# Performance work log

Hardware: AMD Instinct MI355X
Metric: run time of the kernel (lower is better)

Reference implementation:

```python
import jax, jax.numpy as jnp
import numpy as np

B, N, M, C1, C2, H = 16, 4096, 1024, 256, 512, 256
SE_C = max(1, int(H / 24.0))  # 10
BN_EPS = 1e-5

def _bn(x, g, b):
    # training-mode BatchNorm over (B, n) per channel; x: [B, C, n]
    mean = jnp.mean(x, axis=(0, 2), keepdims=True)
    var = jnp.mean((x - mean) ** 2, axis=(0, 2), keepdims=True)  # biased var (torch)
    return (x - mean) * jax.lax.rsqrt(var + BN_EPS) * g[None, :, None] + b[None, :, None]

def _swish(x):
    return x * jax.nn.sigmoid(x)

def setup_inputs() -> dict:
    key = jax.random.key(0)
    ks = jax.random.split(key, 12)
    d = {
        "unknown": jax.random.normal(ks[0], (B, N, 3), jnp.float32),
        "known": jax.random.normal(ks[1], (B, M, 3), jnp.float32),
        "unknow_feats": jax.random.normal(ks[2], (B, C1, N), jnp.float32),
        "known_feats": jax.random.normal(ks[3], (B, C2, M), jnp.float32),
        # conv1 (C1+C2 -> H), no bias (bn)
        "W1": jax.random.normal(ks[4], (H, C1 + C2), jnp.float32) * (1.0 / np.sqrt(C1 + C2)),
        "g1": jnp.ones((H,), jnp.float32),
        "b1": jnp.zeros((H,), jnp.float32),
        # SE block (1x1 convs with bias, no pooling in this impl)
        "se_rw": jax.random.normal(ks[5], (SE_C, H), jnp.float32) * (1.0 / np.sqrt(H)),
        "se_rb": jnp.zeros((SE_C,), jnp.float32),
        "se_ew": jax.random.normal(ks[6], (H, SE_C), jnp.float32) * (1.0 / np.sqrt(SE_C)),
        "se_eb": jnp.zeros((H,), jnp.float32),
        # conv2 (H -> H), no bias
        "W2": jax.random.normal(ks[7], (H, H), jnp.float32) * (1.0 / np.sqrt(H)),
        "g2": jnp.ones((H,), jnp.float32),
        "b2": jnp.zeros((H,), jnp.float32),
    }
    return d

def reference(unknown, known, unknow_feats, known_feats,
              W1, g1, b1, se_rw, se_rb, se_ew, se_eb, W2, g2, b2):
    # three_nn: squared distances of each unknown point to all known points
    d2 = jnp.sum((unknown[:, :, None, :] - known[:, None, :, :]) ** 2, axis=-1)  # [B,N,M]
    neg_d, idx = jax.lax.top_k(-d2, 3)  # 3 smallest
    dist = -neg_d                                       # [B,N,3]
    dist_recip = 1.0 / (dist + 1e-8)
    weight = dist_recip / jnp.sum(dist_recip, axis=2, keepdims=True)  # [B,N,3]
    # three_interpolate: gather known_feats at idx, inverse-distance weighted sum
    gathered = jnp.take_along_axis(known_feats[:, :, None, :], idx[:, None, :, :], axis=3)  # [B,C2,N,3]
    interp = jnp.sum(gathered * weight[:, None, :, :], axis=-1)  # [B,C2,N]
    x = jnp.concatenate([interp, unknow_feats], axis=1)  # [B,C1+C2,N]
    # conv1 (1x1) + BN + SE
    h = jnp.einsum('oc,bcn->bon', W1, x)
    h = _bn(h, g1, b1)
    s = jnp.einsum('oc,bcn->bon', se_rw, h) + se_rb[None, :, None]
    s = _swish(s)
    s = jnp.einsum('oc,bcn->bon', se_ew, s) + se_eb[None, :, None]
    h = jax.nn.sigmoid(s) * h
    # conv2 (1x1) + BN + ReLU
    h = jnp.einsum('oc,bcn->bon', W2, h)
    h = _bn(h, g2, b2)
    return jax.nn.relu(h)  # [B, H, N]
```

## Files before the change

kernel.cpp:

```cpp
#include <hip/hip_runtime.h>
#include <math.h>

#define B_ 16
#define N_ 4096
#define M_ 1024
#define C1_ 256
#define C2_ 512
#define H_ 256
#define SEC_ 10
#define OC_ 8
#define BN_EPS 1e-5f

typedef _Float16 f16;
typedef f16 f16x8 __attribute__((ext_vector_type(8)));
typedef f16 f16x4 __attribute__((ext_vector_type(4)));
typedef f16 f16x2 __attribute__((ext_vector_type(2)));
typedef float f32x4 __attribute__((ext_vector_type(4)));

__global__ __launch_bounds__(256)
void three_nn_kernel(const float* __restrict__ unknown, const float* __restrict__ known,
                     int* __restrict__ idxp, float* __restrict__ wgtp)
{
    __shared__ float kx[M_], ky[M_], kz[M_];
    __shared__ float cd[4][64][3];
    __shared__ int   ci[4][64][3];
    const int b  = blockIdx.y;
    const int bn = blockIdx.x * 64;
    const int t  = threadIdx.x;
    const float* kb = known + (long)b * M_ * 3;

    {
        const float4 q0 = *(const float4*)(kb + 12*t);
        const float4 q1 = *(const float4*)(kb + 12*t + 4);
        const float4 q2 = *(const float4*)(kb + 12*t + 8);
        const int m = 4*t;
        kx[m+0]=q0.x; ky[m+0]=q0.y; kz[m+0]=q0.z;
        kx[m+1]=q0.w; ky[m+1]=q1.x; kz[m+1]=q1.y;
        kx[m+2]=q1.z; ky[m+2]=q1.w; kz[m+2]=q2.x;
        kx[m+3]=q2.y; ky[m+3]=q2.z; kz[m+3]=q2.w;
    }
    __syncthreads();

    const int w = t >> 6, ln = t & 63;
    const int n = bn + ln;
    const float* up = unknown + ((long)b * N_ + n) * 3;
    const float ux = up[0], uy = up[1], uz = up[2];

    float b0 = 1e30f, b1v = 1e30f, b2v = 1e30f;
    int j0 = 0, j1 = 0, j2 = 0;

    const int m0 = w * 256;
    for (int m = m0; m < m0 + 256; m += 4) {
        const float4 X = *(const float4*)&kx[m];
        const float4 Y = *(const float4*)&ky[m];
        const float4 Z = *(const float4*)&kz[m];
        const float px[4] = {X.x, X.y, X.z, X.w};
        const float py[4] = {Y.x, Y.y, Y.z, Y.w};
        const float pz[4] = {Z.x, Z.y, Z.z, Z.w};
        #pragma unroll
        for (int q = 0; q < 4; q++) {
            const float dx = ux - px[q], dy = uy - py[q], dz = uz - pz[q];
            const float d = dx*dx + dy*dy + dz*dz;
            if (d < b2v) {
                const int mm = m + q;
                if (d < b1v) {
                    b2v = b1v; j2 = j1;
                    if (d < b0) { b1v = b0; j1 = j0; b0 = d; j0 = mm; }
                    else        { b1v = d;  j1 = mm; }
                } else { b2v = d; j2 = mm; }
            }
        }
    }
    cd[w][ln][0] = b0;  cd[w][ln][1] = b1v; cd[w][ln][2] = b2v;
    ci[w][ln][0] = j0;  ci[w][ln][1] = j1;  ci[w][ln][2] = j2;
    __syncthreads();

    if (t < 64) {
        float d0 = cd[0][t][0], d1 = cd[0][t][1], d2 = cd[0][t][2];
        int   i0 = ci[0][t][0], i1 = ci[0][t][1], i2 = ci[0][t][2];
        #pragma unroll
        for (int c = 1; c < 4; c++) {
            #pragma unroll
            for (int j = 0; j < 3; j++) {
                const float d = cd[c][t][j];
                const int  ix = ci[c][t][j];
                if (d < d2) {
                    if (d < d1) {
                        d2 = d1; i2 = i1;
                        if (d < d0) { d1 = d0; i1 = i0; d0 = d; i0 = ix; }
                        else        { d1 = d;  i1 = ix; }
                    } else { d2 = d; i2 = ix; }
                }
            }
        }
        const float r0 = 1.f/(d0 + 1e-8f), r1 = 1.f/(d1 + 1e-8f), r2 = 1.f/(d2 + 1e-8f);
        const float rs = 1.f/(r0 + r1 + r2);
        const long base = ((long)b * N_ + bn + t) * 3;
        idxp[base+0] = i0; idxp[base+1] = i1; idxp[base+2] = i2;
        wgtp[base+0] = r0*rs; wgtp[base+1] = r1*rs; wgtp[base+2] = r2*rs;
    }
}

template<int MODE>
__global__ __launch_bounds__(256)
void gemm_mfma(const float* __restrict__ A, int lda,
               const float* __restrict__ Bf, const f16* __restrict__ Bh,
               long strideB, int ldb, int K,
               f16* __restrict__ Ch, long strideC, int ldc,
               const f16* __restrict__ Gt,
               const int* __restrict__ idxp, const float* __restrict__ wgtp,
               float* __restrict__ psum,
               const float* __restrict__ spart, const float* __restrict__ rbAdj,
               const float* __restrict__ se_ewp, const float* __restrict__ se_ebp,
               const float* __restrict__ a1p, const float* __restrict__ c1p)
{
    __shared__ __align__(16) f16 As[256*72];
    __shared__ __align__(16) f16 Bs[64*72];
    __shared__ float sswl[SEC_*64];

    const int b   = blockIdx.z;
    const int bn  = blockIdx.x * 64;
    const int tid = threadIdx.x;
    const int l = tid & 63, w = tid >> 6;
    const int lane16 = l & 15, quad = l >> 4;

    const float* Bfb = nullptr;
    const f16*   Bhb = nullptr;
    if constexpr (MODE == 2) Bhb = Bh + (long)b*strideB;
    else                     Bfb = Bf + (long)b*strideB;

    if constexpr (MODE == 2) {
        for (int i = tid; i < SEC_*64; i += 256) {
            const int j = i >> 6, nn = i & 63;
            float v = rbAdj[j];
            #pragma unroll
            for (int oc = 0; oc < OC_; oc++)
                v += spart[(((long)oc*B_ + b)*SEC_ + j)*N_ + bn + nn];
            sswl[j*64 + nn] = v / (1.f + __expf(-v));
        }
        __syncthreads();
    }

    f32x4 acc[4][4];
    #pragma unroll
    for (int i = 0; i < 4; i++)
        #pragma unroll
        for (int j = 0; j < 4; j++)
            acc[i][j] = (f32x4){0.f, 0.f, 0.f, 0.f};

    const int akb = (tid & 3) * 16;
    const int arw = tid >> 2;

    for (int k0 = 0; k0 < K; k0 += 64) {
        #pragma unroll
        for (int p = 0; p < 4; p++) {
            const int r = p*64 + arw;
            const float* src = A + (long)r*lda + k0 + akb;
            const float4 v0 = *(const float4*)(src);
            const float4 v1 = *(const float4*)(src + 4);
            const float4 v2 = *(const float4*)(src + 8);
            const float4 v3 = *(const float4*)(src + 12);
            f16x8 h0, h1;
            h0[0]=(f16)v0.x; h0[1]=(f16)v0.y; h0[2]=(f16)v0.z; h0[3]=(f16)v0.w;
            h0[4]=(f16)v1.x; h0[5]=(f16)v1.y; h0[6]=(f16)v1.z; h0[7]=(f16)v1.w;
            h1[0]=(f16)v2.x; h1[1]=(f16)v2.y; h1[2]=(f16)v2.z; h1[3]=(f16)v2.w;
            h1[4]=(f16)v3.x; h1[5]=(f16)v3.y; h1[6]=(f16)v3.z; h1[7]=(f16)v3.w;
            *(f16x8*)&As[r*72 + akb]     = h0;
            *(f16x8*)&As[r*72 + akb + 8] = h1;
        }
        #pragma unroll
        for (int it = 0; it < 2; it++) {
            const int slot = it*256 + tid;
            const int k2 = slot >> 4;
            const int n0 = (slot & 15) * 4;
            if constexpr (MODE == 2) {
                const int ka = k0 + 2*k2;
                const f16* s0 = Bhb + (long)ka*ldb + bn + n0;
                const f16x4 ua = *(const f16x4*)s0;
                const f16x4 ub = *(const f16x4*)(s0 + ldb);
                float val[2][4];
                #pragma unroll
                for (int r = 0; r < 2; r++) {
                    const int kr = ka + r;
                    const float aa = a1p[kr], cc = c1p[kr], eb = se_ebp[kr];
                    const float* ew = se_ewp + kr*SEC_;
                    #pragma unroll
                    for (int j = 0; j < 4; j++) {
                        float e = eb;
                        #pragma unroll
                        for (int q = 0; q < SEC_; q++) e += ew[q]*sswl[q*64 + n0 + j];
                        const float g  = 1.f/(1.f + __expf(-e));
                        const float hv = (r == 0) ? (float)ua[j] : (float)ub[j];
                        val[r][j] = g * (aa*hv + cc);
                    }
                }
                #pragma unroll
                for (int j = 0; j < 4; j++) {
                    f16x2 p; p[0] = (f16)val[0][j]; p[1] = (f16)val[1][j];
                    *(f16x2*)&Bs[(n0+j)*72 + 2*k2] = p;
                }
            } else {
                const float* s0 = Bfb + (long)(k0 + 2*k2)*ldb + bn + n0;
                const float4 u = *(const float4*)s0;
                const float4 v = *(const float4*)(s0 + ldb);
                f16x2 p0, p1, p2, p3;
                p0[0]=(f16)u.x; p0[1]=(f16)v.x;
                p1[0]=(f16)u.y; p1[1]=(f16)v.y;
                p2[0]=(f16)u.z; p2[1]=(f16)v.z;
                p3[0]=(f16)u.w; p3[1]=(f16)v.w;
                *(f16x2*)&Bs[(n0+0)*72 + 2*k2] = p0;
                *(f16x2*)&Bs[(n0+1)*72 + 2*k2] = p1;
                *(f16x2*)&Bs[(n0+2)*72 + 2*k2] = p2;
                *(f16x2*)&Bs[(n0+3)*72 + 2*k2] = p3;
            }
        }
        __syncthreads();
        const int abase = (w*64 + lane16)*72 + quad*8;
        const int bbase = lane16*72 + quad*8;
        #pragma unroll
        for (int s = 0; s < 2; s++) {
            f16x8 af[4], bf[4];
            #pragma unroll
            for (int i = 0; i < 4; i++) af[i] = *(const f16x8*)&As[abase + i*1152 + s*32];
            #pragma unroll
            for (int j = 0; j < 4; j++) bf[j] = *(const f16x8*)&Bs[bbase + j*1152 + s*32];
            #pragma unroll
            for (int i = 0; i < 4; i++)
                #pragma unroll
                for (int j = 0; j < 4; j++)
                    acc[i][j] = __builtin_amdgcn_mfma_f32_16x16x32_f16(af[i], bf[j], acc[i][j], 0, 0, 0);
        }
        __syncthreads();
    }

    if constexpr (MODE == 0) {
        f16* Gl = As;
        #pragma unroll
        for (int i = 0; i < 4; i++)
            #pragma unroll
            for (int r = 0; r < 4; r++) {
                const int h = w*64 + i*16 + quad*4 + r;
                #pragma unroll
                for (int j = 0; j < 4; j++)
                    Gl[(j*16 + lane16)*264 + h] = (f16)acc[i][j][r];
            }
        __syncthreads();
        f16* Gtb = Ch + (long)b*strideC + (long)bn*H_;
        #pragma unroll
        for (int it = 0; it < 8; it++) {
            const int t = it*256 + tid;
            const int m = t >> 5, c = (t & 31)*8;
            *(f16x8*)&Gtb[m*H_ + c] = *(const f16x8*)&Gl[m*264 + c];
        }
    } else {
        if constexpr (MODE == 1) {
            f16* P = As;
            const int p  = tid >> 2;
            const int qd = tid & 3;
            const long ib = ((long)b*N_ + bn + p)*3;
            const int i0 = idxp[ib], i1 = idxp[ib+1], i2 = idxp[ib+2];
            const float w0 = wgtp[ib], w1 = wgtp[ib+1], w2 = wgtp[ib+2];
            const f16* gb = Gt + (long)b*M_*H_;
            const f16* g0 = gb + (long)i0*H_ + qd*64;
            const f16* g1 = gb + (long)i1*H_ + qd*64;
            const f16* g2 = gb + (long)i2*H_ + qd*64;
            f16* Pr = P + p*264 + qd*64;
            #pragma unroll
            for (int c = 0; c < 64; c += 8) {
                const f16x8 x0 = *(const f16x8*)&g0[c];
                const f16x8 x1 = *(const f16x8*)&g1[c];
                const f16x8 x2 = *(const f16x8*)&g2[c];
                f16x8 o;
                #pragma unroll
                for (int e = 0; e < 8; e++)
                    o[e] = (f16)(w0*(float)x0[e] + w1*(float)x1[e] + w2*(float)x2[e]);
                *(f16x8*)&Pr[c] = o;
            }
            __syncthreads();
            #pragma unroll
            for (int i = 0; i < 4; i++)
                #pragma unroll
                for (int r = 0; r < 4; r++) {
                    const int h = w*64 + i*16 + quad*4 + r;
                    #pragma unroll
                    for (int j = 0; j < 4; j++)
                        acc[i][j][r] += (float)P[(j*16 + lane16)*264 + h];
                }
        }
        const int bid = blockIdx.z * gridDim.x + blockIdx.x;
        float* ps = psum + (long)bid * (2*H_);
        f16* Cb = Ch + (long)b*strideC;
        #pragma unroll
        for (int i = 0; i < 4; i++)
            #pragma unroll
            for (int r = 0; r < 4; r++) {
                const int row = w*64 + i*16 + quad*4 + r;
                float s1 = 0.f, s2 = 0.f;
                #pragma unroll
                for (int j = 0; j < 4; j++) {
                    const float v = acc[i][j][r];
                    s1 += v; s2 += v*v;
                    Cb[(long)row*ldc + bn + j*16 + lane16] = (f16)v;
                }
                #pragma unroll
                for (int off = 1; off < 16; off <<= 1) {
                    s1 += __shfl_xor(s1, off, 64);
                    s2 += __shfl_xor(s2, off, 64);
                }
                if (lane16 == 0) {
                    ps[row]      = s1;
                    ps[H_ + row] = s2;
                }
            }
    }
}

__global__ __launch_bounds__(256)
void reduce_stats_kernel(const float* __restrict__ psum, float* __restrict__ stats, int nblk)
{
    __shared__ float red[8][33];
    const int o  = blockIdx.x*32 + (threadIdx.x & 31);
    const int ch = threadIdx.x >> 5;
    float s = 0.f;
    for (int bid = ch; bid < nblk; bid += 8)
        s += psum[(long)bid*(2*H_) + o];
    red[ch][threadIdx.x & 31] = s;
    __syncthreads();
    if (ch == 0) {
        float t = 0.f;
        #pragma unroll
        for (int c = 0; c < 8; c++) t += red[c][threadIdx.x & 31];
        stats[o] = t;
    }
}

__global__ __launch_bounds__(256)
void finalize1_kernel(const float* __restrict__ stats,
                      const float* __restrict__ g, const float* __restrict__ bb,
                      const float* __restrict__ se_rw, const float* __restrict__ se_rb,
                      float* __restrict__ a1, float* __restrict__ c1,
                      float* __restrict__ rw2, float* __restrict__ rbAdj)
{
    __shared__ float cbuf[H_];
    __shared__ float red[256];
    const int o = threadIdx.x;
    const float inv = 1.f / (float)(B_ * N_);
    const float S1 = stats[o], S2 = stats[H_ + o];
    const float mean = S1 * inv;
    const float var  = S2 * inv - mean*mean;
    const float a = g[o] * rsqrtf(var + BN_EPS);
    const float c = bb[o] - mean*a;
    a1[o] = a; c1[o] = c; cbuf[o] = c;
    for (int j = 0; j < SEC_; j++) rw2[j*H_ + o] = se_rw[j*H_ + o] * a;
    __syncthreads();
    for (int j = 0; j < SEC_; j++) {
        red[o] = se_rw[j*H_ + o] * cbuf[o];
        __syncthreads();
        for (int s = 128; s > 0; s >>= 1) {
            if (o < s) red[o] += red[o + s];
            __syncthreads();
        }
        if (o == 0) rbAdj[j] = se_rb[j] + red[0];
        __syncthreads();
    }
}

__global__ __launch_bounds__(256)
void se_reduce_kernel(const f16* __restrict__ h1h, const float* __restrict__ rw2,
                      float* __restrict__ spart)
{
    constexpr int OCH = H_ / OC_;
    __shared__ float rwl[SEC_][OCH];
    const int b = blockIdx.y, oc = blockIdx.z;
    const int n0 = blockIdx.x*1024 + threadIdx.x*4;
    for (int i = threadIdx.x; i < SEC_*OCH; i += 256)
        rwl[i/OCH][i%OCH] = rw2[(i/OCH)*H_ + oc*OCH + (i%OCH)];
    __syncthreads();
    f32x4 acc[SEC_];
    #pragma unroll
    for (int j = 0; j < SEC_; j++) acc[j] = (f32x4){0.f,0.f,0.f,0.f};
    const f16* hp = h1h + ((long)b*H_ + oc*OCH)*N_ + n0;
    for (int o = 0; o < OCH; o++) {
        const f16x4 h = *(const f16x4*)(hp + (long)o*N_);
        f32x4 hf; hf[0]=(float)h[0]; hf[1]=(float)h[1]; hf[2]=(float)h[2]; hf[3]=(float)h[3];
        #pragma unroll
        for (int j = 0; j < SEC_; j++) acc[j] += rwl[j][o]*hf;
    }
    #pragma unroll
    for (int j = 0; j < SEC_; j++)
        *(f32x4*)&spart[(((long)oc*B_ + b)*SEC_ + j)*N_ + n0] = acc[j];
}

__global__ __launch_bounds__(256)
void finalize2_kernel(const float* __restrict__ stats,
                      const float* __restrict__ g, const float* __restrict__ bb,
                      float* __restrict__ a2, float* __restrict__ c2)
{
    const int o = threadIdx.x;
    const float inv = 1.f / (float)(B_ * N_);
    const float S1 = stats[o], S2 = stats[H_ + o];
    const float mean = S1 * inv;
    const float var  = S2 * inv - mean*mean;
    const float a = g[o] * rsqrtf(var + BN_EPS);
    a2[o] = a; c2[o] = bb[o] - mean*a;
}

__global__ __launch_bounds__(256)
void bn_relu_kernel(const f16* __restrict__ h2h, float* __restrict__ out,
                    const float* __restrict__ a2, const float* __restrict__ c2)
{
    const long e = ((long)blockIdx.x*256 + threadIdx.x)*8;
    const int o = (int)((e >> 12) & (H_ - 1));
    const f16x8 v = *(const f16x8*)(h2h + e);
    const float a = a2[o], c = c2[o];
    float4 r0, r1;
    r0.x = fmaxf(a*(float)v[0] + c, 0.f);
    r0.y = fmaxf(a*(float)v[1] + c, 0.f);
    r0.z = fmaxf(a*(float)v[2] + c, 0.f);
    r0.w = fmaxf(a*(float)v[3] + c, 0.f);
    r1.x = fmaxf(a*(float)v[4] + c, 0.f);
    r1.y = fmaxf(a*(float)v[5] + c, 0.f);
    r1.z = fmaxf(a*(float)v[6] + c, 0.f);
    r1.w = fmaxf(a*(float)v[7] + c, 0.f);
    *(float4*)(out + e)     = r0;
    *(float4*)(out + e + 4) = r1;
}

extern "C" void kernel_launch(void* const* d_in, const int* in_sizes, int n_in,
                              void* d_out, int out_size, void* d_ws, size_t ws_size,
                              hipStream_t stream)
{
    const float* unknown = (const float*)d_in[0];
    const float* known   = (const float*)d_in[1];
    const float* uf      = (const float*)d_in[2];
    const float* kf      = (const float*)d_in[3];
    const float* W1      = (const float*)d_in[4];
    const float* g1      = (const float*)d_in[5];
    const float* b1      = (const float*)d_in[6];
    const float* se_rw   = (const float*)d_in[7];
    const float* se_rb   = (const float*)d_in[8];
    const float* se_ew   = (const float*)d_in[9];
    const float* se_eb   = (const float*)d_in[10];
    const float* W2      = (const float*)d_in[11];
    const float* g2      = (const float*)d_in[12];
    const float* b2      = (const float*)d_in[13];

    char* ws = (char*)d_ws;
    size_t off = 0;
    auto alloc = [&](size_t bytes) -> void* {
        void* p = ws + off;
        off += (bytes + 255) & ~(size_t)255;
        return p;
    };
    const int NBLK = (N_/64) * B_;
    int*   idxp   = (int*)  alloc((size_t)B_*N_*3*4);
    float* wgtp   = (float*)alloc((size_t)B_*N_*3*4);
    f16*   Gt     = (f16*)  alloc((size_t)B_*M_*H_*2);
    f16*   h1h    = (f16*)  alloc((size_t)B_*H_*N_*2);
    f16*   h2h    = (f16*)  alloc((size_t)B_*H_*N_*2);
    float* spart  = (float*)alloc((size_t)OC_*B_*SEC_*N_*4);
    float* psum1  = (float*)alloc((size_t)NBLK*2*H_*4);
    float* psum2  = (float*)alloc((size_t)NBLK*2*H_*4);
    float* stats1 = (float*)alloc(2*H_*4);
    float* stats2 = (float*)alloc(2*H_*4);
    float* a1     = (float*)alloc(H_*4);
    float* c1     = (float*)alloc(H_*4);
    float* rw2    = (float*)alloc(SEC_*H_*4);
    float* rbAdj  = (float*)alloc(64*4);
    float* a2     = (float*)alloc(H_*4);
    float* c2     = (float*)alloc(H_*4);
    (void)ws_size; (void)in_sizes; (void)n_in; (void)out_size;

    float* out = (float*)d_out;

    three_nn_kernel<<<dim3(N_/64, B_), 256, 0, stream>>>(unknown, known, idxp, wgtp);

    gemm_mfma<0><<<dim3(M_/64, 1, B_), 256, 0, stream>>>(
        W1, C1_+C2_, kf, nullptr, (long)C2_*M_, M_, C2_,
        Gt, (long)M_*H_, 0,
        nullptr, nullptr, nullptr, nullptr,
        nullptr, nullptr, nullptr, nullptr, nullptr, nullptr);

    gemm_mfma<1><<<dim3(N_/64, 1, B_), 256, 0, stream>>>(
        W1 + C2_, C1_+C2_, uf, nullptr, (long)C1_*N_, N_, C1_,
        h1h, (long)H_*N_, N_,
        Gt, idxp, wgtp, psum1,
        nullptr, nullptr, nullptr, nullptr, nullptr, nullptr);

    reduce_stats_kernel<<<dim3(16), 256, 0, stream>>>(psum1, stats1, NBLK);

    finalize1_kernel<<<1, 256, 0, stream>>>(stats1, g1, b1, se_rw, se_rb, a1, c1, rw2, rbAdj);

    se_reduce_kernel<<<dim3(N_/1024, B_, OC_), 256, 0, stream>>>(h1h, rw2, spart);

    gemm_mfma<2><<<dim3(N_/64, 1, B_), 256, 0, stream>>>(
        W2, H_, nullptr, h1h, (long)H_*N_, N_, H_,
        h2h, (long)H_*N_, N_,
        nullptr, nullptr, nullptr, psum2,
        spart, rbAdj, se_ew, se_eb, a1, c1);

    reduce_stats_kernel<<<dim3(16), 256, 0, stream>>>(psum2, stats2, NBLK);

    finalize2_kernel<<<1, 256, 0, stream>>>(stats2, g2, b2, a2, c2);

    bn_relu_kernel<<<dim3((unsigned)((long)B_*H_*N_/2048)), 256, 0, stream>>>(h2h, out, a2, c2);
}
```

Baseline: 446.4 us.

## Pre-convert inputs to fp16 transposed layout and restructure GEMM/SE pipeline

Adds kernels that pre-convert the weights to fp16 and transpose/convert the feature inputs into point-major fp16 layouts. The GEMM is rewritten to stage a full 256-wide K slab of B in LDS and stream A per wave, with point-major outputs. The SE reduction becomes an MFMA kernel followed by a separate in-place gating pass. conv2 now writes fp32 output directly so BN+ReLU runs in place. The aim is to remove per-tile fp32-to-fp16 conversion, strided transposed stores and the heavy SE gating inside the GEMM, at the cost of extra launches and extra transpose traffic.

```diff
diff --git a/kernel.cpp b/kernel.cpp
--- a/kernel.cpp
+++ b/kernel.cpp
@@ -8,14 +8,58 @@
 #define C2_ 512
 #define H_ 256
 #define SEC_ 10
-#define OC_ 8
 #define BN_EPS 1e-5f
 
 typedef _Float16 f16;
 typedef f16 f16x8 __attribute__((ext_vector_type(8)));
 typedef f16 f16x4 __attribute__((ext_vector_type(4)));
-typedef f16 f16x2 __attribute__((ext_vector_type(2)));
 typedef float f32x4 __attribute__((ext_vector_type(4)));
+
+__global__ __launch_bounds__(256)
+void conv_weights_kernel(const float* __restrict__ W1, const float* __restrict__ W2,
+                         f16* __restrict__ W1h, f16* __restrict__ W2h)
+{
+    const int i = (blockIdx.x*256 + threadIdx.x)*4;
+    const int n1 = H_*(C1_+C2_);
+    if (i < n1) {
+        const float4 v = *(const float4*)(W1 + i);
+        f16x4 o; o[0]=(f16)v.x; o[1]=(f16)v.y; o[2]=(f16)v.z; o[3]=(f16)v.w;
+        *(f16x4*)(W1h + i) = o;
+    } else {
+        const int j = i - n1;
+        const float4 v = *(const float4*)(W2 + j);
+        f16x4 o; o[0]=(f16)v.x; o[1]=(f16)v.y; o[2]=(f16)v.z; o[3]=(f16)v.w;
+        *(f16x4*)(W2h + j) = o;
+    }
+}
+
+__global__ __launch_bounds__(256)
+void transpose_cvt_kernel(const float* __restrict__ src, f16* __restrict__ dst,
+                          int Nsrc, int dstStride, long srcBS, long dstBS)
+{
+    __shared__ __align__(16) f16 T[64*264];
+    const int b  = blockIdx.z;
+    const int c0 = blockIdx.y*256;
+    const int n0 = blockIdx.x*64;
+    const int t  = threadIdx.x;
+    {
+        const float* s = src + (long)b*srcBS + (long)(c0 + t)*Nsrc + n0;
+        #pragma unroll
+        for (int i = 0; i < 16; i++) {
+            const float4 v = *(const float4*)(s + i*4);
+            T[(i*4+0)*264 + t] = (f16)v.x;
+            T[(i*4+1)*264 + t] = (f16)v.y;
+            T[(i*4+2)*264 + t] = (f16)v.z;
+            T[(i*4+3)*264 + t] = (f16)v.w;
+        }
+    }
+    __syncthreads();
+    const int n = t >> 2, ch = t & 3;
+    f16* d = dst + (long)b*dstBS + (long)(n0 + n)*dstStride + c0 + ch*64;
+    #pragma unroll
+    for (int i = 0; i < 8; i++)
+        *(f16x8*)(d + i*8) = *(const f16x8*)&T[n*264 + ch*64 + i*8];
+}
 
 __global__ __launch_bounds__(256)
 void three_nn_kernel(const float* __restrict__ unknown, const float* __restrict__ known,
@@ -28,7 +72,6 @@
     const int bn = blockIdx.x * 64;
     const int t  = threadIdx.x;
     const float* kb = known + (long)b * M_ * 3;
-
     {
         const float4 q0 = *(const float4*)(kb + 12*t);
         const float4 q1 = *(const float4*)(kb + 12*t + 4);
@@ -40,15 +83,12 @@
         kx[m+3]=q2.y; ky[m+3]=q2.z; kz[m+3]=q2.w;
     }
     __syncthreads();
-
     const int w = t >> 6, ln = t & 63;
     const int n = bn + ln;
     const float* up = unknown + ((long)b * N_ + n) * 3;
     const float ux = up[0], uy = up[1], uz = up[2];
-
     float b0 = 1e30f, b1v = 1e30f, b2v = 1e30f;
     int j0 = 0, j1 = 0, j2 = 0;
-
     const int m0 = w * 256;
     for (int m = m0; m < m0 + 256; m += 4) {
         const float4 X = *(const float4*)&kx[m];
@@ -74,7 +114,6 @@
     cd[w][ln][0] = b0;  cd[w][ln][1] = b1v; cd[w][ln][2] = b2v;
     ci[w][ln][0] = j0;  ci[w][ln][1] = j1;  ci[w][ln][2] = j2;
     __syncthreads();
-
     if (t < 64) {
         float d0 = cd[0][t][0], d1 = cd[0][t][1], d2 = cd[0][t][2];
         int   i0 = ci[0][t][0], i1 = ci[0][t][1], i2 = ci[0][t][2];
@@ -101,45 +140,28 @@
     }
 }
 
-template<int MODE>
-__global__ __launch_bounds__(256)
-void gemm_mfma(const float* __restrict__ A, int lda,
-               const float* __restrict__ Bf, const f16* __restrict__ Bh,
-               long strideB, int ldb, int K,
-               f16* __restrict__ Ch, long strideC, int ldc,
-               const f16* __restrict__ Gt,
-               const int* __restrict__ idxp, const float* __restrict__ wgtp,
-               float* __restrict__ psum,
-               const float* __restrict__ spart, const float* __restrict__ rbAdj,
-               const float* __restrict__ se_ewp, const float* __restrict__ se_ebp,
-               const float* __restrict__ a1p, const float* __restrict__ c1p)
-{
-    __shared__ __align__(16) f16 As[256*72];
-    __shared__ __align__(16) f16 Bs[64*72];
-    __shared__ float sswl[SEC_*64];
-
-    const int b   = blockIdx.z;
+template<int MODE, int KHN>
+__global__ __launch_bounds__(256)
+void gemm_mfma2(const f16* __restrict__ A, int lda,
+                const f16* __restrict__ Bt, int ldb,
+                f16* __restrict__ Ct, float* __restrict__ outf,
+                const f16* __restrict__ Gt,
+                const int* __restrict__ idxp, const float* __restrict__ wgtp,
+                float* __restrict__ psum)
+{
+    static __shared__ __align__(16) char smem[54272];
+    f16* Bsh = (f16*)smem;
+    f16* Aw  = (f16*)(smem + 33792);
+    f16* P   = (f16*)smem;
+
+    const int b   = blockIdx.y;
     const int bn  = blockIdx.x * 64;
     const int tid = threadIdx.x;
     const int l = tid & 63, w = tid >> 6;
     const int lane16 = l & 15, quad = l >> 4;
-
-    const float* Bfb = nullptr;
-    const f16*   Bhb = nullptr;
-    if constexpr (MODE == 2) Bhb = Bh + (long)b*strideB;
-    else                     Bfb = Bf + (long)b*strideB;
-
-    if constexpr (MODE == 2) {
-        for (int i = tid; i < SEC_*64; i += 256) {
-            const int j = i >> 6, nn = i & 63;
-            float v = rbAdj[j];
-            #pragma unroll
-            for (int oc = 0; oc < OC_; oc++)
-                v += spart[(((long)oc*B_ + b)*SEC_ + j)*N_ + bn + nn];
-            sswl[j*64 + nn] = v / (1.f + __expf(-v));
-        }
-        __syncthreads();
-    }
+    const long nrows = (long)gridDim.x * 64;
+
+    const f16* Bb = Bt + (long)b * nrows * ldb;
 
     f32x4 acc[4][4];
     #pragma unroll
@@ -148,113 +170,67 @@
         for (int j = 0; j < 4; j++)
             acc[i][j] = (f32x4){0.f, 0.f, 0.f, 0.f};
 
-    const int akb = (tid & 3) * 16;
-    const int arw = tid >> 2;
-
-    for (int k0 = 0; k0 < K; k0 += 64) {
-        #pragma unroll
-        for (int p = 0; p < 4; p++) {
-            const int r = p*64 + arw;
-            const float* src = A + (long)r*lda + k0 + akb;
-            const float4 v0 = *(const float4*)(src);
-            const float4 v1 = *(const float4*)(src + 4);
-            const float4 v2 = *(const float4*)(src + 8);
-            const float4 v3 = *(const float4*)(src + 12);
-            f16x8 h0, h1;
-            h0[0]=(f16)v0.x; h0[1]=(f16)v0.y; h0[2]=(f16)v0.z; h0[3]=(f16)v0.w;
-            h0[4]=(f16)v1.x; h0[5]=(f16)v1.y; h0[6]=(f16)v1.z; h0[7]=(f16)v1.w;
-            h1[0]=(f16)v2.x; h1[1]=(f16)v2.y; h1[2]=(f16)v2.z; h1[3]=(f16)v2.w;
-            h1[4]=(f16)v3.x; h1[5]=(f16)v3.y; h1[6]=(f16)v3.z; h1[7]=(f16)v3.w;
-            *(f16x8*)&As[r*72 + akb]     = h0;
-            *(f16x8*)&As[r*72 + akb + 8] = h1;
-        }
-        #pragma unroll
-        for (int it = 0; it < 2; it++) {
-            const int slot = it*256 + tid;
-            const int k2 = slot >> 4;
-            const int n0 = (slot & 15) * 4;
-            if constexpr (MODE == 2) {
-                const int ka = k0 + 2*k2;
-                const f16* s0 = Bhb + (long)ka*ldb + bn + n0;
-                const f16x4 ua = *(const f16x4*)s0;
-                const f16x4 ub = *(const f16x4*)(s0 + ldb);
-                float val[2][4];
-                #pragma unroll
-                for (int r = 0; r < 2; r++) {
-                    const int kr = ka + r;
-                    const float aa = a1p[kr], cc = c1p[kr], eb = se_ebp[kr];
-                    const float* ew = se_ewp + kr*SEC_;
-                    #pragma unroll
-                    for (int j = 0; j < 4; j++) {
-                        float e = eb;
-                        #pragma unroll
-                        for (int q = 0; q < SEC_; q++) e += ew[q]*sswl[q*64 + n0 + j];
-                        const float g  = 1.f/(1.f + __expf(-e));
-                        const float hv = (r == 0) ? (float)ua[j] : (float)ub[j];
-                        val[r][j] = g * (aa*hv + cc);
-                    }
-                }
-                #pragma unroll
-                for (int j = 0; j < 4; j++) {
-                    f16x2 p; p[0] = (f16)val[0][j]; p[1] = (f16)val[1][j];
-                    *(f16x2*)&Bs[(n0+j)*72 + 2*k2] = p;
-                }
-            } else {
-                const float* s0 = Bfb + (long)(k0 + 2*k2)*ldb + bn + n0;
-                const float4 u = *(const float4*)s0;
-                const float4 v = *(const float4*)(s0 + ldb);
-                f16x2 p0, p1, p2, p3;
-                p0[0]=(f16)u.x; p0[1]=(f16)v.x;
-                p1[0]=(f16)u.y; p1[1]=(f16)v.y;
-                p2[0]=(f16)u.z; p2[1]=(f16)v.z;
-                p3[0]=(f16)u.w; p3[1]=(f16)v.w;
-                *(f16x2*)&Bs[(n0+0)*72 + 2*k2] = p0;
-                *(f16x2*)&Bs[(n0+1)*72 + 2*k2] = p1;
-                *(f16x2*)&Bs[(n0+2)*72 + 2*k2] = p2;
-                *(f16x2*)&Bs[(n0+3)*72 + 2*k2] = p3;
-            }
-        }
-        __syncthreads();
-        const int abase = (w*64 + lane16)*72 + quad*8;
-        const int bbase = lane16*72 + quad*8;
-        #pragma unroll
-        for (int s = 0; s < 2; s++) {
+    const int sn = tid >> 2, sc = tid & 3;
+
+    for (int kh = 0; kh < KHN; kh++) {
+        __syncthreads();
+        {
+            const f16* s = Bb + (long)(bn + sn)*ldb + kh*256 + sc*64;
+            f16* d = Bsh + sn*264 + sc*64;
+            #pragma unroll
+            for (int i = 0; i < 8; i++)
+                *(f16x8*)(d + i*8) = *(const f16x8*)(s + i*8);
+        }
+        __syncthreads();
+        const f16* Arow = A + (long)(w*64 + l)*lda + kh*256;
+        f16* Adst = Aw + w*2560 + l*40;
+        f16x8 areg[4];
+        #pragma unroll
+        for (int c = 0; c < 4; c++) areg[c] = *(const f16x8*)(Arow + c*8);
+        #pragma unroll
+        for (int kc = 0; kc < 8; kc++) {
+            #pragma unroll
+            for (int c = 0; c < 4; c++) *(f16x8*)(Adst + c*8) = areg[c];
+            if (kc < 7) {
+                #pragma unroll
+                for (int c = 0; c < 4; c++)
+                    areg[c] = *(const f16x8*)(Arow + (kc+1)*32 + c*8);
+            }
             f16x8 af[4], bf[4];
             #pragma unroll
-            for (int i = 0; i < 4; i++) af[i] = *(const f16x8*)&As[abase + i*1152 + s*32];
-            #pragma unroll
-            for (int j = 0; j < 4; j++) bf[j] = *(const f16x8*)&Bs[bbase + j*1152 + s*32];
+            for (int i = 0; i < 4; i++)
+                af[i] = *(const f16x8*)&Aw[w*2560 + (i*16 + lane16)*40 + quad*8];
+            #pragma unroll
+            for (int j = 0; j < 4; j++)
+                bf[j] = *(const f16x8*)&Bsh[(j*16 + lane16)*264 + kc*32 + quad*8];
             #pragma unroll
             for (int i = 0; i < 4; i++)
                 #pragma unroll
                 for (int j = 0; j < 4; j++)
                     acc[i][j] = __builtin_amdgcn_mfma_f32_16x16x32_f16(af[i], bf[j], acc[i][j], 0, 0, 0);
         }
-        __syncthreads();
-    }
+    }
+
+    __syncthreads();
 
     if constexpr (MODE == 0) {
-        f16* Gl = As;
         #pragma unroll
         for (int i = 0; i < 4; i++)
             #pragma unroll
             for (int r = 0; r < 4; r++) {
-                const int h = w*64 + i*16 + quad*4 + r;
+                const int row = w*64 + i*16 + quad*4 + r;
                 #pragma unroll
                 for (int j = 0; j < 4; j++)
-                    Gl[(j*16 + lane16)*264 + h] = (f16)acc[i][j][r];
-            }
-        __syncthreads();
-        f16* Gtb = Ch + (long)b*strideC + (long)bn*H_;
-        #pragma unroll
-        for (int it = 0; it < 8; it++) {
-            const int t = it*256 + tid;
-            const int m = t >> 5, c = (t & 31)*8;
-            *(f16x8*)&Gtb[m*H_ + c] = *(const f16x8*)&Gl[m*264 + c];
-        }
-    } else {
-        if constexpr (MODE == 1) {
-            f16* P = As;
+                    P[(j*16 + lane16)*264 + row] = (f16)acc[i][j][r];
+            }
+        __syncthreads();
+        const int n = tid >> 2, ch = tid & 3;
+        f16* d = Ct + ((long)b*nrows + bn + n)*256 + ch*64;
+        #pragma unroll
+        for (int i = 0; i < 8; i++)
+            *(f16x8*)(d + i*8) = *(const f16x8*)&P[n*264 + ch*64 + i*8];
+    } else if constexpr (MODE == 1) {
+        {
             const int p  = tid >> 2;
             const int qd = tid & 3;
             const long ib = ((long)b*N_ + bn + p)*3;
@@ -276,20 +252,10 @@
                     o[e] = (f16)(w0*(float)x0[e] + w1*(float)x1[e] + w2*(float)x2[e]);
                 *(f16x8*)&Pr[c] = o;
             }
-            __syncthreads();
-            #pragma unroll
-            for (int i = 0; i < 4; i++)
-                #pragma unroll
-                for (int r = 0; r < 4; r++) {
-                    const int h = w*64 + i*16 + quad*4 + r;
-                    #pragma unroll
-                    for (int j = 0; j < 4; j++)
-                        acc[i][j][r] += (float)P[(j*16 + lane16)*264 + h];
-                }
-        }
-        const int bid = blockIdx.z * gridDim.x + blockIdx.x;
+        }
+        __syncthreads();
+        const int bid = blockIdx.y*gridDim.x + blockIdx.x;
         float* ps = psum + (long)bid * (2*H_);
-        f16* Cb = Ch + (long)b*strideC;
         #pragma unroll
         for (int i = 0; i < 4; i++)
             #pragma unroll
@@ -298,19 +264,46 @@
                 float s1 = 0.f, s2 = 0.f;
                 #pragma unroll
                 for (int j = 0; j < 4; j++) {
-                    const float v = acc[i][j][r];
+                    const int idx = (j*16 + lane16)*264 + row;
+                    const float v = acc[i][j][r] + (float)P[idx];
+                    P[idx] = (f16)v;
                     s1 += v; s2 += v*v;
-                    Cb[(long)row*ldc + bn + j*16 + lane16] = (f16)v;
                 }
                 #pragma unroll
                 for (int off = 1; off < 16; off <<= 1) {
                     s1 += __shfl_xor(s1, off, 64);
                     s2 += __shfl_xor(s2, off, 64);
                 }
-                if (lane16 == 0) {
-                    ps[row]      = s1;
-                    ps[H_ + row] = s2;
+                if (lane16 == 0) { ps[row] = s1; ps[H_ + row] = s2; }
+            }
+        __syncthreads();
+        const int n = tid >> 2, ch = tid & 3;
+        f16* d = Ct + ((long)b*N_ + bn + n)*256 + ch*64;
+        #pragma unroll
+        for (int i = 0; i < 8; i++)
+            *(f16x8*)(d + i*8) = *(const f16x8*)&P[n*264 + ch*64 + i*8];
+    } else {
+        const int bid = blockIdx.y*gridDim.x + blockIdx.x;
+        float* ps = psum + (long)bid * (2*H_);
+        float* Ob = outf + (long)b*H_*N_;
+        #pragma unroll
+        for (int i = 0; i < 4; i++)
+            #pragma unroll
+            for (int r = 0; r < 4; r++) {
+                const int row = w*64 + i*16 + quad*4 + r;
+                float s1 = 0.f, s2 = 0.f;
+                #pragma unroll
+                for (int j = 0; j < 4; j++) {
+                    const float v = acc[i][j][r];
+                    Ob[(long)row*N_ + bn + j*16 + lane16] = v;
+                    s1 += v; s2 += v*v;
                 }
+                #pragma unroll
+                for (int off = 1; off < 16; off <<= 1) {
+                    s1 += __shfl_xor(s1, off, 64);
+                    s2 += __shfl_xor(s2, off, 64);
+                }
+                if (lane16 == 0) { ps[row] = s1; ps[H_ + row] = s2; }
             }
     }
 }
@@ -339,7 +332,7 @@
                       const float* __restrict__ g, const float* __restrict__ bb,
                       const float* __restrict__ se_rw, const float* __restrict__ se_rb,
                       float* __restrict__ a1, float* __restrict__ c1,
-                      float* __restrict__ rw2, float* __restrict__ rbAdj)
+                      f16* __restrict__ rw2h, float* __restrict__ rbAdj)
 {
     __shared__ float cbuf[H_];
     __shared__ float red[256];
@@ -351,7 +344,8 @@
     const float a = g[o] * rsqrtf(var + BN_EPS);
     const float c = bb[o] - mean*a;
     a1[o] = a; c1[o] = c; cbuf[o] = c;
-    for (int j = 0; j < SEC_; j++) rw2[j*H_ + o] = se_rw[j*H_ + o] * a;
+    for (int j = 0; j < SEC_; j++) rw2h[j*H_ + o] = (f16)(se_rw[j*H_ + o] * a);
+    for (int j = SEC_; j < 16; j++) rw2h[j*H_ + o] = (f16)0.f;
     __syncthreads();
     for (int j = 0; j < SEC_; j++) {
         red[o] = se_rw[j*H_ + o] * cbuf[o];
@@ -366,29 +360,59 @@
 }
 
 __global__ __launch_bounds__(256)
-void se_reduce_kernel(const f16* __restrict__ h1h, const float* __restrict__ rw2,
-                      float* __restrict__ spart)
-{
-    constexpr int OCH = H_ / OC_;
-    __shared__ float rwl[SEC_][OCH];
-    const int b = blockIdx.y, oc = blockIdx.z;
-    const int n0 = blockIdx.x*1024 + threadIdx.x*4;
-    for (int i = threadIdx.x; i < SEC_*OCH; i += 256)
-        rwl[i/OCH][i%OCH] = rw2[(i/OCH)*H_ + oc*OCH + (i%OCH)];
-    __syncthreads();
-    f32x4 acc[SEC_];
+void se_mfma_kernel(const f16* __restrict__ h1t, const f16* __restrict__ rw2h,
+                    const float* __restrict__ rbAdj, float* __restrict__ ssw)
+{
+    const int b = blockIdx.y, bn = blockIdx.x*64;
+    const int t = threadIdx.x, w = t >> 6, l = t & 63;
+    const int lane16 = l & 15, quad = l >> 4;
+    const int n0 = bn + w*16;
+    f32x4 acc = (f32x4){0.f,0.f,0.f,0.f};
+    const f16* hb = h1t + ((long)b*N_ + n0 + lane16)*256;
     #pragma unroll
-    for (int j = 0; j < SEC_; j++) acc[j] = (f32x4){0.f,0.f,0.f,0.f};
-    const f16* hp = h1h + ((long)b*H_ + oc*OCH)*N_ + n0;
-    for (int o = 0; o < OCH; o++) {
-        const f16x4 h = *(const f16x4*)(hp + (long)o*N_);
-        f32x4 hf; hf[0]=(float)h[0]; hf[1]=(float)h[1]; hf[2]=(float)h[2]; hf[3]=(float)h[3];
-        #pragma unroll
-        for (int j = 0; j < SEC_; j++) acc[j] += rwl[j][o]*hf;
-    }
+    for (int kc = 0; kc < 8; kc++) {
+        const f16x8 a  = *(const f16x8*)&rw2h[lane16*256 + kc*32 + quad*8];
+        const f16x8 bf = *(const f16x8*)&hb[kc*32 + quad*8];
+        acc = __builtin_amdgcn_mfma_f32_16x16x32_f16(a, bf, acc, 0, 0, 0);
+    }
+    const int nn = n0 + lane16;
     #pragma unroll
-    for (int j = 0; j < SEC_; j++)
-        *(f32x4*)&spart[(((long)oc*B_ + b)*SEC_ + j)*N_ + n0] = acc[j];
+    for (int r = 0; r < 4; r++) {
+        const int j = quad*4 + r;
+        if (j < SEC_) {
+            const float s = acc[r] + rbAdj[j];
+            ssw[((long)b*N_ + nn)*SEC_ + j] = s / (1.f + __expf(-s));
+        }
+    }
+}
+
+__global__ __launch_bounds__(256)
+void h1g_kernel(f16* __restrict__ h1t, const float* __restrict__ ssw,
+                const float* __restrict__ se_ew, const float* __restrict__ se_eb,
+                const float* __restrict__ a1, const float* __restrict__ c1)
+{
+    const int t = threadIdx.x;
+    const long n = (long)blockIdx.x*128 + (t & 127);
+    const int half = t >> 7;
+    float sswr[SEC_];
+    #pragma unroll
+    for (int j = 0; j < SEC_; j++) sswr[j] = ssw[n*SEC_ + j];
+    f16* row = h1t + n*256 + half*128;
+    #pragma unroll
+    for (int i = 0; i < 16; i++) {
+        f16x8 h = *(f16x8*)&row[i*8];
+        f16x8 o;
+        #pragma unroll
+        for (int e = 0; e < 8; e++) {
+            const int k = half*128 + i*8 + e;
+            float ev = se_eb[k];
+            #pragma unroll
+            for (int j = 0; j < SEC_; j++) ev += se_ew[k*SEC_ + j]*sswr[j];
+            const float gg = 1.f/(1.f + __expf(-ev));
+            o[e] = (f16)(gg*(a1[k]*(float)h[e] + c1[k]));
+        }
+        *(f16x8*)&row[i*8] = o;
+    }
 }
 
 __global__ __launch_bounds__(256)
@@ -406,24 +430,18 @@
 }
 
 __global__ __launch_bounds__(256)
-void bn_relu_kernel(const f16* __restrict__ h2h, float* __restrict__ out,
-                    const float* __restrict__ a2, const float* __restrict__ c2)
-{
-    const long e = ((long)blockIdx.x*256 + threadIdx.x)*8;
+void bn_relu_kernel(float* __restrict__ out, const float* __restrict__ a2,
+                    const float* __restrict__ c2)
+{
+    const long e = ((long)blockIdx.x*256 + threadIdx.x)*4;
     const int o = (int)((e >> 12) & (H_ - 1));
-    const f16x8 v = *(const f16x8*)(h2h + e);
+    float4 v = *(float4*)(out + e);
     const float a = a2[o], c = c2[o];
-    float4 r0, r1;
-    r0.x = fmaxf(a*(float)v[0] + c, 0.f);
-    r0.y = fmaxf(a*(float)v[1] + c, 0.f);
-    r0.z = fmaxf(a*(float)v[2] + c, 0.f);
-    r0.w = fmaxf(a*(float)v[3] + c, 0.f);
-    r1.x = fmaxf(a*(float)v[4] + c, 0.f);
-    r1.y = fmaxf(a*(float)v[5] + c, 0.f);
-    r1.z = fmaxf(a*(float)v[6] + c, 0.f);
-    r1.w = fmaxf(a*(float)v[7] + c, 0.f);
-    *(float4*)(out + e)     = r0;
-    *(float4*)(out + e + 4) = r1;
+    v.x = fmaxf(a*v.x + c, 0.f);
+    v.y = fmaxf(a*v.y + c, 0.f);
+    v.z = fmaxf(a*v.z + c, 0.f);
+    v.w = fmaxf(a*v.w + c, 0.f);
+    *(float4*)(out + e) = v;
 }
 
 extern "C" void kernel_launch(void* const* d_in, const int* in_sizes, int n_in,
@@ -455,17 +473,20 @@
     const int NBLK = (N_/64) * B_;
     int*   idxp   = (int*)  alloc((size_t)B_*N_*3*4);
     float* wgtp   = (float*)alloc((size_t)B_*N_*3*4);
+    f16*   W1h    = (f16*)  alloc((size_t)H_*(C1_+C2_)*2);
+    f16*   W2h    = (f16*)  alloc((size_t)H_*H_*2);
+    f16*   uft    = (f16*)  alloc((size_t)B_*N_*C1_*2);
+    f16*   kft    = (f16*)  alloc((size_t)B_*M_*C2_*2);
     f16*   Gt     = (f16*)  alloc((size_t)B_*M_*H_*2);
-    f16*   h1h    = (f16*)  alloc((size_t)B_*H_*N_*2);
-    f16*   h2h    = (f16*)  alloc((size_t)B_*H_*N_*2);
-    float* spart  = (float*)alloc((size_t)OC_*B_*SEC_*N_*4);
+    f16*   h1t    = (f16*)  alloc((size_t)B_*N_*H_*2);
+    float* ssw    = (float*)alloc((size_t)B_*N_*SEC_*4);
     float* psum1  = (float*)alloc((size_t)NBLK*2*H_*4);
     float* psum2  = (float*)alloc((size_t)NBLK*2*H_*4);
     float* stats1 = (float*)alloc(2*H_*4);
     float* stats2 = (float*)alloc(2*H_*4);
     float* a1     = (float*)alloc(H_*4);
     float* c1     = (float*)alloc(H_*4);
-    float* rw2    = (float*)alloc(SEC_*H_*4);
+    f16*   rw2h   = (f16*)  alloc(16*H_*2);
     float* rbAdj  = (float*)alloc(64*4);
     float* a2     = (float*)alloc(H_*4);
     float* c2     = (float*)alloc(H_*4);
@@ -473,35 +494,32 @@
 
     float* out = (float*)d_out;
 
+    conv_weights_kernel<<<dim3(256), 256, 0, stream>>>(W1, W2, W1h, W2h);
+    transpose_cvt_kernel<<<dim3(N_/64, 1, B_), 256, 0, stream>>>(
+        uf, uft, N_, C1_, (long)C1_*N_, (long)N_*C1_);
+    transpose_cvt_kernel<<<dim3(M_/64, 2, B_), 256, 0, stream>>>(
+        kf, kft, M_, C2_, (long)C2_*M_, (long)M_*C2_);
+
     three_nn_kernel<<<dim3(N_/64, B_), 256, 0, stream>>>(unknown, known, idxp, wgtp);
 
-    gemm_mfma<0><<<dim3(M_/64, 1, B_), 256, 0, stream>>>(
-        W1, C1_+C2_, kf, nullptr, (long)C2_*M_, M_, C2_,
-        Gt, (long)M_*H_, 0,
-        nullptr, nullptr, nullptr, nullptr,
-        nullptr, nullptr, nullptr, nullptr, nullptr, nullptr);
-
-    gemm_mfma<1><<<dim3(N_/64, 1, B_), 256, 0, stream>>>(
-        W1 + C2_, C1_+C2_, uf, nullptr, (long)C1_*N_, N_, C1_,
-        h1h, (long)H_*N_, N_,
-        Gt, idxp, wgtp, psum1,
-        nullptr, nullptr, nullptr, nullptr, nullptr, nullptr);
+    gemm_mfma2<0,2><<<dim3(M_/64, B_), 256, 0, stream>>>(
+        W1h, C1_+C2_, kft, C2_, Gt, nullptr, nullptr, nullptr, nullptr, nullptr);
+
+    gemm_mfma2<1,1><<<dim3(N_/64, B_), 256, 0, stream>>>(
+        W1h + C2_, C1_+C2_, uft, C1_, h1t, nullptr, Gt, idxp, wgtp, psum1);
 
     reduce_stats_kernel<<<dim3(16), 256, 0, stream>>>(psum1, stats1, NBLK);
-
-    finalize1_kernel<<<1, 256, 0, stream>>>(stats1, g1, b1, se_rw, se_rb, a1, c1, rw2, rbAdj);
-
-    se_reduce_kernel<<<dim3(N_/1024, B_, OC_), 256, 0, stream>>>(h1h, rw2, spart);
-
-    gemm_mfma<2><<<dim3(N_/64, 1, B_), 256, 0, stream>>>(
-        W2, H_, nullptr, h1h, (long)H_*N_, N_, H_,
-        h2h, (long)H_*N_, N_,
-        nullptr, nullptr, nullptr, psum2,
-        spart, rbAdj, se_ew, se_eb, a1, c1);
+    finalize1_kernel<<<1, 256, 0, stream>>>(stats1, g1, b1, se_rw, se_rb, a1, c1, rw2h, rbAdj);
+
+    se_mfma_kernel<<<dim3(N_/64, B_), 256, 0, stream>>>(h1t, rw2h, rbAdj, ssw);
+
+    h1g_kernel<<<dim3(B_*N_/128), 256, 0, stream>>>(h1t, ssw, se_ew, se_eb, a1, c1);
+
+    gemm_mfma2<2,1><<<dim3(N_/64, B_), 256, 0, stream>>>(
+        W2h, H_, h1t, H_, nullptr, out, nullptr, nullptr, nullptr, psum2);
 
     reduce_stats_kernel<<<dim3(16), 256, 0, stream>>>(psum2, stats2, NBLK);
-
     finalize2_kernel<<<1, 256, 0, stream>>>(stats2, g2, b2, a2, c2);
 
-    bn_relu_kernel<<<dim3((unsigned)((long)B_*H_*N_/2048)), 256, 0, stream>>>(h2h, out, a2, c2);
-}
+    bn_relu_kernel<<<dim3((unsigned)((long)B_*H_*N_/1024)), 256, 0, stream>>>(out, a2, c2);
+}
```

After: 514.5 us. 15.2% more time.
